# Kernel optimization log

Hardware: AMD Instinct MI355X
Metric: run time of the kernel (lower is better)

Reference implementation:

```python
import jax, jax.numpy as jnp
import numpy as np

L, B, S, D, H, V, F = 4, 2, 2048, 1024, 16, 50257, 4096
DH = D // H

def _ln(x, w, b):
    m = x.mean(-1, keepdims=True)
    v = ((x - m) ** 2).mean(-1, keepdims=True)
    return (x - m) / jnp.sqrt(v + 1e-5) * w + b

def _rope(x):
    # x: [B, H, S, DH]; xformers-style half-split rotation
    dh = x.shape[-1]
    inv = 1.0 / (10000.0 ** (jnp.arange(0, dh, 2, dtype=jnp.float32) / dh))
    t = jnp.arange(x.shape[-2], dtype=jnp.float32)
    fr = t[:, None] * inv[None, :]                      # [S, DH/2]
    emb = jnp.concatenate([fr, fr], axis=-1)            # [S, DH]
    cos, sin = jnp.cos(emb), jnp.sin(emb)
    x1, x2 = jnp.split(x, 2, axis=-1)
    return x * cos + jnp.concatenate([-x2, x1], axis=-1) * sin

def setup_inputs() -> dict:
    key = jax.random.key(0)
    ks = jax.random.split(key, 12)
    d = {}
    d['tokens'] = jax.random.randint(ks[0], (B, S), 0, V)
    d['targets'] = jax.random.randint(ks[1], (B, S), 0, V)
    d['word_emb'] = jax.random.normal(ks[2], (V, D), jnp.float32) * 0.02
    d['pos_emb'] = jax.random.normal(ks[3], (S, D), jnp.float32) * 0.02
    d['ln1_w'] = jnp.ones((L, D), jnp.float32)
    d['ln1_b'] = jnp.zeros((L, D), jnp.float32)
    d['wq'] = jax.random.normal(ks[4], (L, D, D), jnp.float32) * 0.02
    d['bq'] = jnp.zeros((L, D), jnp.float32)
    d['wk'] = jax.random.normal(ks[5], (L, D, D), jnp.float32) * 0.02
    d['bk'] = jnp.zeros((L, D), jnp.float32)
    d['wv'] = jax.random.normal(ks[6], (L, D, D), jnp.float32) * 0.02
    d['bv'] = jnp.zeros((L, D), jnp.float32)
    d['wo'] = jax.random.normal(ks[7], (L, D, D), jnp.float32) * 0.02
    d['bo'] = jnp.zeros((L, D), jnp.float32)
    d['ln2_w'] = jnp.ones((L, D), jnp.float32)
    d['ln2_b'] = jnp.zeros((L, D), jnp.float32)
    d['w1'] = jax.random.normal(ks[8], (L, D, F), jnp.float32) * 0.02
    d['b1'] = jnp.zeros((L, F), jnp.float32)
    d['w2'] = jax.random.normal(ks[9], (L, F, D), jnp.float32) * 0.02
    d['b2'] = jnp.zeros((L, D), jnp.float32)
    d['post_w'] = jnp.ones((D,), jnp.float32)
    d['post_b'] = jnp.zeros((D,), jnp.float32)
    d['lnf_w'] = jnp.ones((D,), jnp.float32)
    d['lnf_b'] = jnp.zeros((D,), jnp.float32)
    d['head_w'] = jax.random.normal(ks[10], (D, V), jnp.float32) * 0.02
    return d

def reference(tokens, targets, word_emb, pos_emb, ln1_w, ln1_b, wq, bq, wk, bk, wv, bv, wo, bo, ln2_w, ln2_b, w1, b1, w2, b2, post_w, post_b, lnf_w, lnf_b, head_w):
    # first encoder's VocabEmbedding: token + learned positional embedding
    x = word_emb[tokens] + pos_emb[None, :S, :]
    mask = jnp.tril(jnp.ones((S, S), dtype=bool))
    scale = 1.0 / float(np.sqrt(DH))
    for i in range(L):
        # pre-norm block-sparse (tril layout == exact causal) attention with RoPE
        h = _ln(x, ln1_w[i], ln1_b[i])
        q = (h @ wq[i] + bq[i]).reshape(B, S, H, DH).transpose(0, 2, 1, 3)
        k = (h @ wk[i] + bk[i]).reshape(B, S, H, DH).transpose(0, 2, 1, 3)
        v = (h @ wv[i] + bv[i]).reshape(B, S, H, DH).transpose(0, 2, 1, 3)
        q, k = _rope(q), _rope(k)
        scores = jnp.einsum('bhqd,bhkd->bhqk', q, k) * scale
        scores = jnp.where(mask, scores, jnp.float32(-1e9))
        att = jax.nn.softmax(scores, axis=-1)
        o = jnp.einsum('bhqk,bhkd->bhqd', att, v).transpose(0, 2, 1, 3).reshape(B, S, D)
        x = x + o @ wo[i] + bo[i]
        # pre-norm MLP
        h2 = _ln(x, ln2_w[i], ln2_b[i])
        x = x + jax.nn.gelu(h2 @ w1[i] + b1[i], approximate=False) @ w2[i] + b2[i]
        if i == L - 1:
            # last encoder block's FF gets an extra Post-norm wrapper
            x = _ln(x, post_w, post_b)
    x = _ln(x, lnf_w, lnf_b)
    logits = x @ head_w                                  # [B, S, V]
    logp = jax.nn.log_softmax(logits, axis=-1)
    nll = -jnp.take_along_axis(logp, targets[..., None], axis=-1)[..., 0]
    return nll.mean()
```

## Files before the change

kernel.cpp:

```cpp
#include <hip/hip_runtime.h>
#include <hip/hip_bf16.h>
#include <math.h>
#include <stdint.h>

constexpr int Lc  = 4;
constexpr int Bc  = 2;
constexpr int Sc  = 2048;
constexpr int Dc  = 1024;
constexpr int Hc  = 16;
constexpr int Vc  = 50257;
constexpr int Fc  = 4096;
constexpr int DHc = 64;
constexpr int Mr  = Bc * Sc;
constexpr int QKVN = 3 * Dc;
constexpr int Vpad = 50304;
constexpr int NVT  = Vpad / 128;
constexpr int NQT  = Sc / 128;

typedef __attribute__((ext_vector_type(8))) short short8;
typedef __attribute__((ext_vector_type(4))) float f32x4;

__device__ __forceinline__ void gl2lds16(const __hip_bfloat16* g, __hip_bfloat16* l) {
    __builtin_amdgcn_global_load_lds(
        (const uint32_t __attribute__((address_space(1)))*)g,
        (uint32_t __attribute__((address_space(3)))*)l, 16, 0, 0);
}

__device__ __forceinline__ void lse_combine(float& m, float& s, float mo, float so) {
    float mn = fmaxf(m, mo);
    s = s * expf(m - mn) + so * expf(mo - mn);
    m = mn;
}

__global__ void embed_kernel(const int* __restrict__ tokens,
                             const float* __restrict__ we,
                             const float* __restrict__ pe,
                             float* __restrict__ x) {
    int row = blockIdx.x;
    int s   = row & (Sc - 1);
    int tok = tokens[row];
    const float* wp = we + (size_t)tok * Dc;
    const float* pp = pe + (size_t)s * Dc;
    float* xp = x + (size_t)row * Dc;
    for (int i = threadIdx.x; i < Dc; i += blockDim.x)
        xp[i] = wp[i] + pp[i];
}

__global__ __launch_bounds__(256) void ln_kernel(const float* __restrict__ x,
                                                 const float* __restrict__ w,
                                                 const float* __restrict__ b,
                                                 float* __restrict__ outF,
                                                 __hip_bfloat16* __restrict__ outB) {
    __shared__ float red[256];
    int row = blockIdx.x;
    int tid = threadIdx.x;
    const float* xp = x + (size_t)row * Dc;
    float s1 = 0.f, s2 = 0.f;
    for (int i = tid; i < Dc; i += 256) {
        float v = xp[i];
        s1 += v; s2 += v * v;
    }
    red[tid] = s1; __syncthreads();
    for (int off = 128; off > 0; off >>= 1) {
        if (tid < off) red[tid] += red[tid + off];
        __syncthreads();
    }
    float mean = red[0] * (1.0f / Dc);
    __syncthreads();
    red[tid] = s2; __syncthreads();
    for (int off = 128; off > 0; off >>= 1) {
        if (tid < off) red[tid] += red[tid + off];
        __syncthreads();
    }
    float var  = red[0] * (1.0f / Dc) - mean * mean;
    float rstd = rsqrtf(var + 1e-5f);
    for (int i = tid; i < Dc; i += 256) {
        float v = (xp[i] - mean) * rstd * w[i] + b[i];
        if (outF) outF[(size_t)row * Dc + i] = v;
        if (outB) outB[(size_t)row * Dc + i] = __float2bfloat16(v);
    }
}

__global__ __launch_bounds__(256) void convw_kernel(const float* __restrict__ W,
                                                    __hip_bfloat16* __restrict__ Wt,
                                                    int K, int srcN) {
    __shared__ float t[32][33];
    int n0 = blockIdx.x * 32, k0 = blockIdx.y * 32;
    int tx = threadIdx.x & 31, ty = threadIdx.x >> 5;
    #pragma unroll
    for (int j = 0; j < 4; j++) {
        int k = k0 + ty + j * 8, n = n0 + tx;
        t[ty + j * 8][tx] = (n < srcN) ? W[(size_t)k * srcN + n] : 0.f;
    }
    __syncthreads();
    #pragma unroll
    for (int j = 0; j < 4; j++) {
        int n = n0 + ty + j * 8, k = k0 + tx;
        Wt[(size_t)n * K + k] = __float2bfloat16(t[tx][ty + j * 8]);
    }
}

__global__ void bcat_kernel(const float* __restrict__ bq, const float* __restrict__ bk,
                            const float* __restrict__ bv, float* __restrict__ o) {
    int i = blockIdx.x * 256 + threadIdx.x;
    if (i < QKVN)
        o[i] = (i < Dc) ? bq[i] : (i < 2 * Dc) ? bk[i - Dc] : bv[i - 2 * Dc];
}

__global__ __launch_bounds__(256) void bgemm_kernel(
    const __hip_bfloat16* __restrict__ A,
    const __hip_bfloat16* __restrict__ Bt,
    const float* __restrict__ bias,
    const float* __restrict__ Cin,
    float* __restrict__ outF,
    __hip_bfloat16* __restrict__ outB,
    int N, int K, int act) {
    __shared__ __align__(16) __hip_bfloat16 As[128 * 32];
    __shared__ __align__(16) __hip_bfloat16 Bs[128 * 32];
    const int tid = threadIdx.x;
    const int rowBase = blockIdx.y * 128;
    const int colBase = blockIdx.x * 128;
    const int w = tid >> 6, lane = tid & 63;
    const int wm = w >> 1, wn = w & 1;
    const int quad = lane >> 4, l16 = lane & 15;

    f32x4 acc[4][4];
    #pragma unroll
    for (int i = 0; i < 4; i++)
        #pragma unroll
        for (int j = 0; j < 4; j++) acc[i][j] = (f32x4){0.f, 0.f, 0.f, 0.f};

    const __hip_bfloat16* a0 = A  + (size_t)(rowBase + (tid >> 2)) * K + (tid & 3) * 8;
    const __hip_bfloat16* b0 = Bt + (size_t)(colBase + (tid >> 2)) * K + (tid & 3) * 8;
    const size_t rstep = (size_t)64 * K;
    __hip_bfloat16* lA = As + tid * 8;
    __hip_bfloat16* lB = Bs + tid * 8;

    for (int k0 = 0; k0 < K; k0 += 32) {
        __syncthreads();
        gl2lds16(a0 + k0,         lA);
        gl2lds16(a0 + k0 + rstep, lA + 2048);
        gl2lds16(b0 + k0,         lB);
        gl2lds16(b0 + k0 + rstep, lB + 2048);
        __syncthreads();

        short8 af[4], bf[4];
        #pragma unroll
        for (int i = 0; i < 4; i++) {
            af[i] = *(const short8*)(As + (wm * 64 + i * 16 + l16) * 32 + quad * 8);
            bf[i] = *(const short8*)(Bs + (wn * 64 + i * 16 + l16) * 32 + quad * 8);
        }
        #pragma unroll
        for (int i = 0; i < 4; i++)
            #pragma unroll
            for (int j = 0; j < 4; j++)
                acc[i][j] = __builtin_amdgcn_mfma_f32_16x16x32_bf16(af[i], bf[j], acc[i][j], 0, 0, 0);
    }

    #pragma unroll
    for (int i = 0; i < 4; i++) {
        #pragma unroll
        for (int j = 0; j < 4; j++) {
            int col = colBase + wn * 64 + j * 16 + l16;
            float bb = bias ? bias[col] : 0.f;
            #pragma unroll
            for (int r = 0; r < 4; r++) {
                int row = rowBase + wm * 64 + i * 16 + quad * 4 + r;
                float v = acc[i][j][r] + bb;
                if (Cin) v += Cin[(size_t)row * N + col];
                if (act) v = 0.5f * v * (1.0f + erff(v * 0.70710678118654752f));
                if (outF) outF[(size_t)row * N + col] = v;
                if (outB) outB[(size_t)row * N + col] = __float2bfloat16(v);
            }
        }
    }
}

__global__ __launch_bounds__(256) void headgemm_kernel(
    const __hip_bfloat16* __restrict__ A,
    const __hip_bfloat16* __restrict__ Bt,
    const int* __restrict__ targets,
    float* __restrict__ pmax, float* __restrict__ psum,
    float* __restrict__ tlog) {
    __shared__ __align__(16) __hip_bfloat16 As[128 * 32];
    __shared__ __align__(16) __hip_bfloat16 Bs[128 * 32];
    __shared__ float pmW[2][128], psW[2][128];
    __shared__ int tg[128];
    const int tid = threadIdx.x;
    const int rowBase = blockIdx.y * 128;
    const int colBase = blockIdx.x * 128;
    const int K = Dc;
    const int w = tid >> 6, lane = tid & 63;
    const int wm = w >> 1, wn = w & 1;
    const int quad = lane >> 4, l16 = lane & 15;

    if (tid < 128) tg[tid] = targets[rowBase + tid];

    f32x4 acc[4][4];
    #pragma unroll
    for (int i = 0; i < 4; i++)
        #pragma unroll
        for (int j = 0; j < 4; j++) acc[i][j] = (f32x4){0.f, 0.f, 0.f, 0.f};

    const __hip_bfloat16* a0 = A  + (size_t)(rowBase + (tid >> 2)) * K + (tid & 3) * 8;
    const __hip_bfloat16* b0 = Bt + (size_t)(colBase + (tid >> 2)) * K + (tid & 3) * 8;
    const size_t rstep = (size_t)64 * K;
    __hip_bfloat16* lA = As + tid * 8;
    __hip_bfloat16* lB = Bs + tid * 8;

    for (int k0 = 0; k0 < K; k0 += 32) {
        __syncthreads();
        gl2lds16(a0 + k0,         lA);
        gl2lds16(a0 + k0 + rstep, lA + 2048);
        gl2lds16(b0 + k0,         lB);
        gl2lds16(b0 + k0 + rstep, lB + 2048);
        __syncthreads();

        short8 af[4], bf[4];
        #pragma unroll
        for (int i = 0; i < 4; i++) {
            af[i] = *(const short8*)(As + (wm * 64 + i * 16 + l16) * 32 + quad * 8);
            bf[i] = *(const short8*)(Bs + (wn * 64 + i * 16 + l16) * 32 + quad * 8);
        }
        #pragma unroll
        for (int i = 0; i < 4; i++)
            #pragma unroll
            for (int j = 0; j < 4; j++)
                acc[i][j] = __builtin_amdgcn_mfma_f32_16x16x32_bf16(af[i], bf[j], acc[i][j], 0, 0, 0);
    }

    #pragma unroll
    for (int i = 0; i < 4; i++) {
        #pragma unroll
        for (int r = 0; r < 4; r++) {
            int rib = wm * 64 + i * 16 + quad * 4 + r;
            float m = -1e30f, s = 0.f;
            float vals[4];
            #pragma unroll
            for (int j = 0; j < 4; j++) {
                int col = colBase + wn * 64 + j * 16 + l16;
                float v = acc[i][j][r];
                bool ok = (col < Vc);
                if (ok && col == tg[rib]) tlog[rowBase + rib] = v;
                vals[j] = ok ? v : -1e30f;
                m = fmaxf(m, vals[j]);
            }
            #pragma unroll
            for (int j = 0; j < 4; j++) s += expf(vals[j] - m);
            #pragma unroll
            for (int d = 1; d < 16; d <<= 1) {
                float mo = __shfl_xor(m, d, 64);
                float so = __shfl_xor(s, d, 64);
                lse_combine(m, s, mo, so);
            }
            if (l16 == 0) { pmW[wn][rib] = m; psW[wn][rib] = s; }
        }
    }
    __syncthreads();
    if (tid < 128) {
        float m = pmW[0][tid], s = psW[0][tid];
        lse_combine(m, s, pmW[1][tid], psW[1][tid]);
        pmax[(size_t)blockIdx.x * Mr + rowBase + tid] = m;
        psum[(size_t)blockIdx.x * Mr + rowBase + tid] = s;
    }
}

__global__ __launch_bounds__(256) void head_reduce_kernel(
    const float* __restrict__ pmax, const float* __restrict__ psum,
    const float* __restrict__ tlog, float* __restrict__ nll) {
    __shared__ float rm[256], rs[256];
    int row = blockIdx.x;
    int tid = threadIdx.x;
    float m = -1e30f, s = 0.f;
    for (int t = tid; t < NVT; t += 256)
        lse_combine(m, s, pmax[(size_t)t * Mr + row], psum[(size_t)t * Mr + row]);
    rm[tid] = m; rs[tid] = s; __syncthreads();
    for (int off = 128; off > 0; off >>= 1) {
        if (tid < off) {
            float mm = rm[tid], ss = rs[tid];
            lse_combine(mm, ss, rm[tid + off], rs[tid + off]);
            rm[tid] = mm; rs[tid] = ss;
        }
        __syncthreads();
    }
    if (tid == 0) nll[row] = rm[0] + logf(rs[0]) - tlog[row];
}

__global__ void ropecvt_kernel(const __hip_bfloat16* __restrict__ qkvb,
                               __hip_bfloat16* __restrict__ qb,
                               __hip_bfloat16* __restrict__ kb) {
    int p = blockIdx.x * blockDim.x + threadIdx.x;
    if (p >= Mr * Hc * 32) return;
    int j    = p & 31;
    int h    = (p >> 5) & (Hc - 1);
    int srow = p >> 9;
    int s    = srow & (Sc - 1);
    int b    = srow >> 11;
    float inv = powf(10000.0f, -(float)(2 * j) * (1.0f / 64.0f));
    float fr  = (float)s * inv;
    float c = cosf(fr), sn = sinf(fr);
    size_t base = (size_t)srow * QKVN + h * DHc;
    size_t o = ((size_t)(b * Hc + h) * Sc + s) * DHc;
    float q1 = __bfloat162float(qkvb[base + j]);
    float q2 = __bfloat162float(qkvb[base + j + 32]);
    qb[o + j]      = __float2bfloat16((q1 * c - q2 * sn) * 0.125f);
    qb[o + j + 32] = __float2bfloat16((q2 * c + q1 * sn) * 0.125f);
    float k1 = __bfloat162float(qkvb[base + Dc + j]);
    float k2 = __bfloat162float(qkvb[base + Dc + j + 32]);
    kb[o + j]      = __float2bfloat16(k1 * c - k2 * sn);
    kb[o + j + 32] = __float2bfloat16(k2 * c + k1 * sn);
}

__global__ __launch_bounds__(256) void vt_kernel(const __hip_bfloat16* __restrict__ qkvb,
                                                 __hip_bfloat16* __restrict__ vtb) {
    __shared__ float t[32][33];
    int s0 = blockIdx.x * 32, d0 = blockIdx.y * 32;
    int bh = blockIdx.z;
    int b = bh >> 4, h = bh & (Hc - 1);
    int tx = threadIdx.x & 31, ty = threadIdx.x >> 5;
    #pragma unroll
    for (int jj = 0; jj < 4; jj++) {
        int s = s0 + ty + jj * 8;
        t[ty + jj * 8][tx] = __bfloat162float(
            qkvb[((size_t)(b * Sc + s)) * QKVN + 2 * Dc + h * DHc + d0 + tx]);
    }
    __syncthreads();
    #pragma unroll
    for (int jj = 0; jj < 4; jj++) {
        int d = d0 + ty + jj * 8;
        vtb[((size_t)bh * DHc + d) * Sc + s0 + tx] = __float2bfloat16(t[tx][ty + jj * 8]);
    }
}

__global__ __launch_bounds__(256) void attn_mfma_kernel(
    const __hip_bfloat16* __restrict__ qb,
    const __hip_bfloat16* __restrict__ kb,
    const __hip_bfloat16* __restrict__ vtb,
    __hip_bfloat16* __restrict__ ob) {
    __shared__ __align__(16) __hip_bfloat16 Ks[128 * 64];
    __shared__ __align__(16) __hip_bfloat16 Vts[64 * 128];
    __shared__ __align__(16) __hip_bfloat16 Ps[128 * 128];

    const int tid  = threadIdx.x;
    const int idx  = blockIdx.x;
    const int qt   = (NQT - 1) - (idx >> 5);
    const int bh   = idx & 31;
    const int b    = bh >> 4, h = bh & (Hc - 1);
    const int w    = tid >> 6, lane = tid & 63;
    const int quad = lane >> 4, l16 = lane & 15;
    const int sz   = l16 & 7;

    const __hip_bfloat16* kb_bh = kb  + (size_t)bh * Sc * DHc;
    const __hip_bfloat16* vt_bh = vtb + (size_t)bh * DHc * Sc;

    short8 afq[2][2];
    {
        const __hip_bfloat16* qp =
            qb + ((size_t)bh * Sc + qt * 128 + w * 32 + l16) * DHc;
        #pragma unroll
        for (int i = 0; i < 2; i++)
            #pragma unroll
            for (int dc = 0; dc < 2; dc++)
                afq[i][dc] = *(const short8*)(qp + i * 16 * DHc + (dc * 4 + quad) * 8);
    }

    f32x4 oacc[2][4];
    float m[2][4], lsum[2][4];
    #pragma unroll
    for (int i = 0; i < 2; i++)
        #pragma unroll
        for (int dt = 0; dt < 4; dt++) oacc[i][dt] = (f32x4){0.f, 0.f, 0.f, 0.f};
    #pragma unroll
    for (int i = 0; i < 2; i++)
        #pragma unroll
        for (int r = 0; r < 4; r++) { m[i][r] = -1e30f; lsum[i][r] = 0.f; }

    for (int kt = 0; kt <= qt; ++kt) {
        __syncthreads();
        #pragma unroll
        for (int p = 0; p < 4; p++) {
            int k = p * 32 + (tid >> 3);
            gl2lds16(kb_bh + ((size_t)(kt * 128 + k)) * DHc + (((tid & 7) ^ (k & 7)) << 3),
                     Ks + p * 2048 + tid * 8);
        }
        #pragma unroll
        for (int p = 0; p < 4; p++) {
            int d = p * 16 + (tid >> 4);
            gl2lds16(vt_bh + (size_t)d * Sc + kt * 128 + (((tid & 15) ^ (d & 7)) << 3),
                     Vts + p * 2048 + tid * 8);
        }
        __syncthreads();

        f32x4 sacc[2][8];
        #pragma unroll
        for (int i = 0; i < 2; i++)
            #pragma unroll
            for (int j = 0; j < 8; j++) sacc[i][j] = (f32x4){0.f, 0.f, 0.f, 0.f};
        #pragma unroll
        for (int j = 0; j < 8; j++) {
            const __hip_bfloat16* kp = Ks + (j * 16 + l16) * DHc;
            short8 bk0 = *(const short8*)(kp + ((quad ^ sz) << 3));
            short8 bk1 = *(const short8*)(kp + (((4 + quad) ^ sz) << 3));
            #pragma unroll
            for (int i = 0; i < 2; i++) {
                sacc[i][j] = __builtin_amdgcn_mfma_f32_16x16x32_bf16(afq[i][0], bk0, sacc[i][j], 0, 0, 0);
                sacc[i][j] = __builtin_amdgcn_mfma_f32_16x16x32_bf16(afq[i][1], bk1, sacc[i][j], 0, 0, 0);
            }
        }

        const bool diag = (kt == qt);
        #pragma unroll
        for (int i = 0; i < 2; i++) {
            #pragma unroll
            for (int r = 0; r < 4; r++) {
                int rowq = w * 32 + i * 16 + quad * 4 + r;
                float rm = -1e30f;
                #pragma unroll
                for (int j = 0; j < 8; j++) {
                    float v = sacc[i][j][r];
                    if (diag && (j * 16 + l16 > rowq)) v = -1e30f;
                    sacc[i][j][r] = v;
                    rm = fmaxf(rm, v);
                }
                #pragma unroll
                for (int dlt = 1; dlt < 16; dlt <<= 1)
                    rm = fmaxf(rm, __shfl_xor(rm, dlt, 64));
                float mn = fmaxf(m[i][r], rm);
                float fm = __expf(m[i][r] - mn);
                m[i][r] = mn;
                float rs = 0.f;
                #pragma unroll
                for (int j = 0; j < 8; j++) {
                    float pe = __expf(sacc[i][j][r] - mn);
                    sacc[i][j][r] = pe;
                    rs += pe;
                }
                #pragma unroll
                for (int dlt = 1; dlt < 16; dlt <<= 1)
                    rs += __shfl_xor(rs, dlt, 64);
                lsum[i][r] = lsum[i][r] * fm + rs;
                #pragma unroll
                for (int dt = 0; dt < 4; dt++) oacc[i][dt][r] *= fm;
            }
        }

        #pragma unroll
        for (int i = 0; i < 2; i++) {
            #pragma unroll
            for (int r = 0; r < 4; r++) {
                int Q = w * 32 + i * 16 + quad * 4 + r;
                int rowoff = Q * 128;
                int swz = (Q & 7) << 3;
                #pragma unroll
                for (int j = 0; j < 8; j++)
                    Ps[rowoff + ((j * 16 + l16) ^ swz)] = __float2bfloat16(sacc[i][j][r]);
            }
        }

        #pragma unroll
        for (int kc = 0; kc < 4; kc++) {
            int ch = ((kc * 4 + quad) ^ sz) << 3;
            short8 ap[2], bv[4];
            #pragma unroll
            for (int i = 0; i < 2; i++)
                ap[i] = *(const short8*)(Ps + (w * 32 + i * 16 + l16) * 128 + ch);
            #pragma unroll
            for (int dt = 0; dt < 4; dt++)
                bv[dt] = *(const short8*)(Vts + (dt * 16 + l16) * 128 + ch);
            #pragma unroll
            for (int i = 0; i < 2; i++)
                #pragma unroll
                for (int dt = 0; dt < 4; dt++)
                    oacc[i][dt] = __builtin_amdgcn_mfma_f32_16x16x32_bf16(ap[i], bv[dt], oacc[i][dt], 0, 0, 0);
        }
    }

    #pragma unroll
    for (int i = 0; i < 2; i++) {
        #pragma unroll
        for (int r = 0; r < 4; r++) {
            float inv = 1.0f / lsum[i][r];
            int s = qt * 128 + w * 32 + i * 16 + quad * 4 + r;
            size_t base = ((size_t)b * Sc + s) * Dc + h * DHc;
            #pragma unroll
            for (int dt = 0; dt < 4; dt++)
                ob[base + dt * 16 + l16] = __float2bfloat16(oacc[i][dt][r] * inv);
        }
    }
}

__global__ __launch_bounds__(256) void loss_kernel(const float* __restrict__ nll,
                                                   float* __restrict__ out) {
    __shared__ float red[256];
    int tid = threadIdx.x;
    float s = 0.f;
    for (int i = tid; i < Mr; i += 256) s += nll[i];
    red[tid] = s; __syncthreads();
    for (int off = 128; off > 0; off >>= 1) {
        if (tid < off) red[tid] += red[tid + off];
        __syncthreads();
    }
    if (tid == 0) out[0] = red[0] * (1.0f / Mr);
}

extern "C" void kernel_launch(void* const* d_in, const int* in_sizes, int n_in,
                              void* d_out, int out_size, void* d_ws, size_t ws_size,
                              hipStream_t stream) {
    const int*   tokens   = (const int*)  d_in[0];
    const int*   targets  = (const int*)  d_in[1];
    const float* word_emb = (const float*)d_in[2];
    const float* pos_emb  = (const float*)d_in[3];
    const float* ln1_w    = (const float*)d_in[4];
    const float* ln1_b    = (const float*)d_in[5];
    const float* wq       = (const float*)d_in[6];
    const float* bq       = (const float*)d_in[7];
    const float* wk       = (const float*)d_in[8];
    const float* bk       = (const float*)d_in[9];
    const float* wv       = (const float*)d_in[10];
    const float* bv       = (const float*)d_in[11];
    const float* wo       = (const float*)d_in[12];
    const float* bo       = (const float*)d_in[13];
    const float* ln2_w    = (const float*)d_in[14];
    const float* ln2_b    = (const float*)d_in[15];
    const float* w1       = (const float*)d_in[16];
    const float* b1       = (const float*)d_in[17];
    const float* w2       = (const float*)d_in[18];
    const float* b2       = (const float*)d_in[19];
    const float* post_w   = (const float*)d_in[20];
    const float* post_b   = (const float*)d_in[21];
    const float* lnf_w    = (const float*)d_in[22];
    const float* lnf_b    = (const float*)d_in[23];
    const float* head_w   = (const float*)d_in[24];

    float* cur = (float*)d_ws;
    float* x    = cur; cur += (size_t)Mr * Dc;
    float* nll  = cur; cur += Mr;
    float* tlog = cur; cur += Mr;
    float* bqkv = cur; cur += QKVN;
    float* pmax = cur; cur += (size_t)NVT * Mr;
    float* psum = cur; cur += (size_t)NVT * Mr;
    __hip_bfloat16* bcur = (__hip_bfloat16*)cur;
    __hip_bfloat16* hb     = bcur; bcur += (size_t)Mr * Dc;
    __hip_bfloat16* ob     = bcur; bcur += (size_t)Mr * Dc;
    __hip_bfloat16* midb   = bcur; bcur += (size_t)Mr * Fc;
    __hip_bfloat16* qkvb   = bcur; bcur += (size_t)Mr * QKVN;
    __hip_bfloat16* qb     = bcur; bcur += (size_t)Mr * Dc;
    __hip_bfloat16* kbuf   = bcur; bcur += (size_t)Mr * Dc;
    __hip_bfloat16* Wqkv_t = bcur; bcur += (size_t)QKVN * Dc;
    __hip_bfloat16* Wo_t   = bcur; bcur += (size_t)Dc * Dc;
    __hip_bfloat16* W1_t   = bcur; bcur += (size_t)Fc * Dc;
    __hip_bfloat16* W2_t   = bcur; bcur += (size_t)Dc * Fc;
    __hip_bfloat16* Wh_t   = bcur; bcur += (size_t)Vpad * Dc;
    __hip_bfloat16* vtb = midb;

    dim3 blk(256);

    embed_kernel<<<Mr, blk, 0, stream>>>(tokens, word_emb, pos_emb, x);
    convw_kernel<<<dim3(Vpad / 32, Dc / 32), blk, 0, stream>>>(head_w, Wh_t, Dc, Vc);

    for (int l = 0; l < Lc; l++) {
        convw_kernel<<<dim3(Dc / 32, Dc / 32), blk, 0, stream>>>(wq + (size_t)l * Dc * Dc, Wqkv_t, Dc, Dc);
        convw_kernel<<<dim3(Dc / 32, Dc / 32), blk, 0, stream>>>(wk + (size_t)l * Dc * Dc, Wqkv_t + (size_t)Dc * Dc, Dc, Dc);
        convw_kernel<<<dim3(Dc / 32, Dc / 32), blk, 0, stream>>>(wv + (size_t)l * Dc * Dc, Wqkv_t + (size_t)2 * Dc * Dc, Dc, Dc);
        bcat_kernel<<<QKVN / 256, blk, 0, stream>>>(bq + l * Dc, bk + l * Dc, bv + l * Dc, bqkv);

        ln_kernel<<<Mr, blk, 0, stream>>>(x, ln1_w + l * Dc, ln1_b + l * Dc, nullptr, hb);
        bgemm_kernel<<<dim3(QKVN / 128, Mr / 128), blk, 0, stream>>>(
            hb, Wqkv_t, bqkv, nullptr, nullptr, qkvb, QKVN, Dc, 0);
        ropecvt_kernel<<<(Mr * Hc * 32) / 256, blk, 0, stream>>>(qkvb, qb, kbuf);
        vt_kernel<<<dim3(Sc / 32, DHc / 32, Bc * Hc), blk, 0, stream>>>(qkvb, vtb);
        attn_mfma_kernel<<<Bc * Hc * NQT, blk, 0, stream>>>(qb, kbuf, vtb, ob);

        convw_kernel<<<dim3(Dc / 32, Dc / 32), blk, 0, stream>>>(wo + (size_t)l * Dc * Dc, Wo_t, Dc, Dc);
        bgemm_kernel<<<dim3(Dc / 128, Mr / 128), blk, 0, stream>>>(
            ob, Wo_t, bo + l * Dc, x, x, nullptr, Dc, Dc, 0);

        ln_kernel<<<Mr, blk, 0, stream>>>(x, ln2_w + l * Dc, ln2_b + l * Dc, nullptr, hb);
        convw_kernel<<<dim3(Fc / 32, Dc / 32), blk, 0, stream>>>(w1 + (size_t)l * Dc * Fc, W1_t, Dc, Fc);
        bgemm_kernel<<<dim3(Fc / 128, Mr / 128), blk, 0, stream>>>(
            hb, W1_t, b1 + l * Fc, nullptr, nullptr, midb, Fc, Dc, 1);
        convw_kernel<<<dim3(Dc / 32, Fc / 32), blk, 0, stream>>>(w2 + (size_t)l * Fc * Dc, W2_t, Fc, Dc);
        bgemm_kernel<<<dim3(Dc / 128, Mr / 128), blk, 0, stream>>>(
            midb, W2_t, b2 + l * Dc, x, x, nullptr, Dc, Fc, 0);

        if (l == Lc - 1)
            ln_kernel<<<Mr, blk, 0, stream>>>(x, post_w, post_b, x, nullptr);
    }

    ln_kernel<<<Mr, blk, 0, stream>>>(x, lnf_w, lnf_b, nullptr, hb);
    headgemm_kernel<<<dim3(NVT, Mr / 128), blk, 0, stream>>>(hb, Wh_t, targets, pmax, psum, tlog);
    head_reduce_kernel<<<Mr, blk, 0, stream>>>(pmax, psum, tlog, nll);
    loss_kernel<<<1, blk, 0, stream>>>(nll, (float*)d_out);
}
```

Baseline: 3.130 ms.

## Swizzle GEMM block order for L2 reuse and use fast GELU/exp in epilogues

Result: faster. 2.974 ms (-5.0%).

```diff
diff --git a/kernel.cpp b/kernel.cpp
--- a/kernel.cpp
+++ b/kernel.cpp
@@ -16,6 +16,7 @@
 constexpr int Vpad = 50304;
 constexpr int NVT  = Vpad / 128;
 constexpr int NQT  = Sc / 128;
+constexpr int NSuperH = (NVT + 7) / 8;
 
 typedef __attribute__((ext_vector_type(8))) short short8;
 typedef __attribute__((ext_vector_type(4))) float f32x4;
@@ -28,8 +29,19 @@
 
 __device__ __forceinline__ void lse_combine(float& m, float& s, float mo, float so) {
     float mn = fmaxf(m, mo);
-    s = s * expf(m - mn) + so * expf(mo - mn);
+    s = s * __expf(m - mn) + so * __expf(mo - mn);
     m = mn;
+}
+
+__device__ __forceinline__ float fast_gelu(float v) {
+    float x  = v * 0.70710678118654752f;
+    float ax = fabsf(x);
+    float t  = 1.0f / (1.0f + 0.3275911f * ax);
+    float y  = t * (0.254829592f + t * (-0.284496736f + t * (1.421413741f +
+               t * (-1.453152027f + t * 1.061405429f))));
+    float erfv = 1.0f - y * __expf(-ax * ax);
+    erfv = (x < 0.f) ? -erfv : erfv;
+    return 0.5f * v * (1.0f + erfv);
 }
 
 __global__ void embed_kernel(const int* __restrict__ tokens,
@@ -118,8 +130,10 @@
     __shared__ __align__(16) __hip_bfloat16 As[128 * 32];
     __shared__ __align__(16) __hip_bfloat16 Bs[128 * 32];
     const int tid = threadIdx.x;
-    const int rowBase = blockIdx.y * 128;
-    const int colBase = blockIdx.x * 128;
+    const int bid = blockIdx.x;
+    const int sup = bid >> 8, wblk = bid & 255;
+    const int rowBase = (wblk & 31) * 128;
+    const int colBase = (sup * 8 + (wblk >> 5)) * 128;
     const int w = tid >> 6, lane = tid & 63;
     const int wm = w >> 1, wn = w & 1;
     const int quad = lane >> 4, l16 = lane & 15;
@@ -168,7 +182,7 @@
                 int row = rowBase + wm * 64 + i * 16 + quad * 4 + r;
                 float v = acc[i][j][r] + bb;
                 if (Cin) v += Cin[(size_t)row * N + col];
-                if (act) v = 0.5f * v * (1.0f + erff(v * 0.70710678118654752f));
+                if (act) v = fast_gelu(v);
                 if (outF) outF[(size_t)row * N + col] = v;
                 if (outB) outB[(size_t)row * N + col] = __float2bfloat16(v);
             }
@@ -187,8 +201,12 @@
     __shared__ float pmW[2][128], psW[2][128];
     __shared__ int tg[128];
     const int tid = threadIdx.x;
-    const int rowBase = blockIdx.y * 128;
-    const int colBase = blockIdx.x * 128;
+    const int bid = blockIdx.x;
+    const int sup = bid >> 8, wblk = bid & 255;
+    const int rowBase = (wblk & 31) * 128;
+    const int colT = sup * 8 + (wblk >> 5);
+    if (colT >= NVT) return;
+    const int colBase = colT * 128;
     const int K = Dc;
     const int w = tid >> 6, lane = tid & 63;
     const int wm = w >> 1, wn = w & 1;
@@ -234,25 +252,27 @@
         #pragma unroll
         for (int r = 0; r < 4; r++) {
             int rib = wm * 64 + i * 16 + quad * 4 + r;
-            float m = -1e30f, s = 0.f;
+            int tgt = tg[rib];
             float vals[4];
+            float m = -1e30f;
             #pragma unroll
             for (int j = 0; j < 4; j++) {
                 int col = colBase + wn * 64 + j * 16 + l16;
                 float v = acc[i][j][r];
                 bool ok = (col < Vc);
-                if (ok && col == tg[rib]) tlog[rowBase + rib] = v;
+                if (ok && col == tgt) tlog[rowBase + rib] = v;
                 vals[j] = ok ? v : -1e30f;
                 m = fmaxf(m, vals[j]);
             }
             #pragma unroll
-            for (int j = 0; j < 4; j++) s += expf(vals[j] - m);
-            #pragma unroll
-            for (int d = 1; d < 16; d <<= 1) {
-                float mo = __shfl_xor(m, d, 64);
-                float so = __shfl_xor(s, d, 64);
-                lse_combine(m, s, mo, so);
-            }
+            for (int d = 1; d < 16; d <<= 1)
+                m = fmaxf(m, __shfl_xor(m, d, 64));
+            float s = 0.f;
+            #pragma unroll
+            for (int j = 0; j < 4; j++) s += __expf(vals[j] - m);
+            #pragma unroll
+            for (int d = 1; d < 16; d <<= 1)
+                s += __shfl_xor(s, d, 64);
             if (l16 == 0) { pmW[wn][rib] = m; psW[wn][rib] = s; }
         }
     }
@@ -260,8 +280,8 @@
     if (tid < 128) {
         float m = pmW[0][tid], s = psW[0][tid];
         lse_combine(m, s, pmW[1][tid], psW[1][tid]);
-        pmax[(size_t)blockIdx.x * Mr + rowBase + tid] = m;
-        psum[(size_t)blockIdx.x * Mr + rowBase + tid] = s;
+        pmax[(size_t)colT * Mr + rowBase + tid] = m;
+        psum[(size_t)colT * Mr + rowBase + tid] = s;
     }
 }
 
@@ -565,22 +585,22 @@
         bcat_kernel<<<QKVN / 256, blk, 0, stream>>>(bq + l * Dc, bk + l * Dc, bv + l * Dc, bqkv);
 
         ln_kernel<<<Mr, blk, 0, stream>>>(x, ln1_w + l * Dc, ln1_b + l * Dc, nullptr, hb);
-        bgemm_kernel<<<dim3(QKVN / 128, Mr / 128), blk, 0, stream>>>(
+        bgemm_kernel<<<(QKVN / 1024) * 256, blk, 0, stream>>>(
             hb, Wqkv_t, bqkv, nullptr, nullptr, qkvb, QKVN, Dc, 0);
         ropecvt_kernel<<<(Mr * Hc * 32) / 256, blk, 0, stream>>>(qkvb, qb, kbuf);
         vt_kernel<<<dim3(Sc / 32, DHc / 32, Bc * Hc), blk, 0, stream>>>(qkvb, vtb);
         attn_mfma_kernel<<<Bc * Hc * NQT, blk, 0, stream>>>(qb, kbuf, vtb, ob);
 
         convw_kernel<<<dim3(Dc / 32, Dc / 32), blk, 0, stream>>>(wo + (size_t)l * Dc * Dc, Wo_t, Dc, Dc);
-        bgemm_kernel<<<dim3(Dc / 128, Mr / 128), blk, 0, stream>>>(
+        bgemm_kernel<<<(Dc / 1024) * 256, blk, 0, stream>>>(
             ob, Wo_t, bo + l * Dc, x, x, nullptr, Dc, Dc, 0);
 
         ln_kernel<<<Mr, blk, 0, stream>>>(x, ln2_w + l * Dc, ln2_b + l * Dc, nullptr, hb);
         convw_kernel<<<dim3(Fc / 32, Dc / 32), blk, 0, stream>>>(w1 + (size_t)l * Dc * Fc, W1_t, Dc, Fc);
-        bgemm_kernel<<<dim3(Fc / 128, Mr / 128), blk, 0, stream>>>(
+        bgemm_kernel<<<(Fc / 1024) * 256, blk, 0, stream>>>(
             hb, W1_t, b1 + l * Fc, nullptr, nullptr, midb, Fc, Dc, 1);
         convw_kernel<<<dim3(Dc / 32, Fc / 32), blk, 0, stream>>>(w2 + (size_t)l * Fc * Dc, W2_t, Fc, Dc);
-        bgemm_kernel<<<dim3(Dc / 128, Mr / 128), blk, 0, stream>>>(
+        bgemm_kernel<<<(Dc / 1024) * 256, blk, 0, stream>>>(
             midb, W2_t, b2 + l * Dc, x, x, nullptr, Dc, Fc, 0);
 
         if (l == Lc - 1)
@@ -588,7 +608,7 @@
     }
 
     ln_kernel<<<Mr, blk, 0, stream>>>(x, lnf_w, lnf_b, nullptr, hb);
-    headgemm_kernel<<<dim3(NVT, Mr / 128), blk, 0, stream>>>(hb, Wh_t, targets, pmax, psum, tlog);
+    headgemm_kernel<<<NSuperH * 256, blk, 0, stream>>>(hb, Wh_t, targets, pmax, psum, tlog);
     head_reduce_kernel<<<Mr, blk, 0, stream>>>(pmax, psum, tlog, nll);
     loss_kernel<<<1, blk, 0, stream>>>(nll, (float*)d_out);
 }
```
